# Performance work log

Hardware: AMD Instinct MI355X
Metric: run time of the kernel (lower is better)

## Reference

```python
import jax, jax.numpy as jnp
import numpy as np

B, C, W, H = 16, 512, 32, 32
CQ = C // 2
WSCALE = 0.05  # keep energy logits in a sane range for softmax


def setup_inputs() -> dict:
    key = jax.random.key(0)
    ks = jax.random.split(key, 6)
    return {
        "x": jax.random.normal(ks[0], (B, C, W, H), dtype=jnp.float32),
        "Wq": jax.random.normal(ks[1], (CQ, C), dtype=jnp.float32) * WSCALE,
        "bq": jnp.zeros((CQ,), dtype=jnp.float32),
        "Wk": jax.random.normal(ks[2], (CQ, C), dtype=jnp.float32) * WSCALE,
        "bk": jnp.zeros((CQ,), dtype=jnp.float32),
        "Wv": jax.random.normal(ks[3], (C, C), dtype=jnp.float32) * WSCALE,
        "bv": jnp.zeros((C,), dtype=jnp.float32),
        "Wa": jax.random.normal(ks[4], (1, C), dtype=jnp.float32) * WSCALE,
        "ba": jnp.zeros((1,), dtype=jnp.float32),
        "gamma": jax.random.normal(ks[5], (1,), dtype=jnp.float32) * 0.1,
    }


def reference(x, Wq, bq, Wk, bk, Wv, bv, Wa, ba, gamma):
    b, c, w, h = x.shape
    n = w * h
    xf = x.reshape(b, c, n)  # flatten spatial: B,C,N
    # 1x1 convs == per-position channel matmuls
    q = jnp.einsum('oc,bcn->bon', Wq, xf) + bq[None, :, None]  # B,C/2,N
    k = jnp.einsum('oc,bcn->bon', Wk, xf) + bk[None, :, None]  # B,C/2,N
    v = jnp.einsum('oc,bcn->bon', Wv, xf) + bv[None, :, None]  # B,C,N
    # energy[b,i,j] = <q[:, i], k[:, j]>  (unscaled, single head)
    energy = jnp.einsum('bci,bcj->bij', q, k)  # B,N,N
    attn = jax.nn.softmax(energy, axis=-1)
    # out[b,c,i] = sum_j v[b,c,j] * attn[b,i,j]
    out = jnp.einsum('bcj,bij->bci', v, attn).reshape(b, c, w, h)
    # agnostic gating: 1x1 conv C->1 + sigmoid, gate = 1 - sigmoid
    ag = jax.nn.sigmoid(jnp.einsum('oc,bchw->bohw', Wa, out) + ba[None, :, None, None])
    out_A = out * (1.0 - ag)
    out_final = gamma[0] * out + x
    return (out_final, out_A)
```

## Files before the change

### kernel.cpp

```cpp
#include <hip/hip_runtime.h>
#include <hip/hip_bf16.h>
#include <math.h>

#define B 16
#define C 512
#define CQ 256
#define N 1024

typedef short bf16x8 __attribute__((ext_vector_type(8)));
typedef _Float16 f16x8 __attribute__((ext_vector_type(8)));
typedef float f32x4 __attribute__((ext_vector_type(4)));
typedef unsigned short ushort;

__device__ __forceinline__ unsigned short f2bf(float f) {
    __hip_bfloat16 h = __float2bfloat16(f);
    return *(unsigned short*)&h;
}
__device__ __forceinline__ ushort f2h(float f) {
    _Float16 h = (_Float16)f;
    return *(ushort*)&h;
}
__device__ __forceinline__ float h2f(ushort u) {
    _Float16 h = *(_Float16*)&u;
    return (float)h;
}
__device__ __forceinline__ f16x8 as_h(bf16x8 v) {
    union { bf16x8 s; f16x8 h; } u; u.s = v; return u.h;
}

__device__ __forceinline__ void gload16(void* lds, const void* g) {
    __builtin_amdgcn_global_load_lds(
        (const __attribute__((address_space(1))) void*)g,
        (__attribute__((address_space(3))) void*)lds, 16, 0, 0);
}

__device__ __forceinline__ void barrier_lgkm() {
    asm volatile("s_waitcnt lgkmcnt(0)" ::: "memory");
    __builtin_amdgcn_s_barrier();
    __builtin_amdgcn_sched_barrier(0);
}

template<int OUT_MODE, int BIAS_MODE, int XSWZ, int DT>
__global__ __launch_bounds__(256) void gemm128s(
    const ushort* __restrict__ A, long long sA,
    const ushort* __restrict__ BT, long long sB,
    void* __restrict__ Ch, long long sC,
    const float* __restrict__ bias, int K, int Ncols)
{
    __shared__ __align__(16) ushort As[128 * 128];
    __shared__ __align__(16) ushort Bs[128 * 128];

    int bx, by, bz;
    if constexpr (XSWZ) {
        const int lin  = blockIdx.x + gridDim.x * (blockIdx.y + gridDim.y * blockIdx.z);
        const int xcd  = lin & 7;
        const int slot = lin >> 3;
        bz = xcd + 8 * (slot >> 5);
        const int wxy = slot & 31;
        bx = wxy % gridDim.x;
        by = wxy / gridDim.x;
    } else {
        bx = blockIdx.x; by = blockIdx.y; bz = blockIdx.z;
    }

    const int tid  = threadIdx.x;
    const int lane = tid & 63;
    const int w    = tid >> 6;
    const int wr   = (w >> 1) * 64;
    const int wc   = (w & 1) * 64;
    const int fr   = lane & 15;
    const int ko2  = (lane >> 4) * 16;

    const int brow = by * 128;
    const int bcol = bx * 128;
    const size_t K2 = (size_t)K * 2;

    const char* Ab = (const char*)(A  + (size_t)bz * sA + (size_t)brow * K);
    const char* Bb = (const char*)(BT + (size_t)bz * sB + (size_t)bcol * K);

    const int sr = tid >> 4;
    const int ss = (tid & 15) * 16;

    f32x4 acc[4][4] = {};

    for (int k0 = 0; k0 < K; k0 += 128) {
#pragma unroll
        for (int p = 0; p < 8; ++p) {
            const int row = p * 16 + sr;
            const size_t so = (size_t)row * K2 + (size_t)k0 * 2
                            + (size_t)(ss ^ ((row & 15) << 4));
            gload16((char*)As + p * 4096 + tid * 16, Ab + so);
            gload16((char*)Bs + p * 4096 + tid * 16, Bb + so);
        }
        __syncthreads();
#pragma unroll
        for (int k32 = 0; k32 < 4; ++k32) {
            const int kswz = (k32 * 64 + ko2) ^ (fr << 4);
            bf16x8 ah[4], bh[4];
#pragma unroll
            for (int m = 0; m < 4; ++m)
                ah[m] = *(const bf16x8*)((const char*)As + (wr + m * 16 + fr) * 256 + kswz);
#pragma unroll
            for (int n = 0; n < 4; ++n)
                bh[n] = *(const bf16x8*)((const char*)Bs + (wc + n * 16 + fr) * 256 + kswz);
            if constexpr (DT == 1) {
#pragma unroll
                for (int m = 0; m < 4; ++m)
#pragma unroll
                    for (int n = 0; n < 4; ++n)
                        acc[m][n] = __builtin_amdgcn_mfma_f32_16x16x32_f16(
                            as_h(ah[m]), as_h(bh[n]), acc[m][n], 0, 0, 0);
            } else {
#pragma unroll
                for (int m = 0; m < 4; ++m)
#pragma unroll
                    for (int n = 0; n < 4; ++n)
                        acc[m][n] = __builtin_amdgcn_mfma_f32_16x16x32_bf16(
                            ah[m], bh[n], acc[m][n], 0, 0, 0);
            }
        }
        __syncthreads();
    }

    const int crow = brow + wr + (lane >> 4) * 4;
    const int ccol = bcol + wc + fr;
    const size_t cbase = (size_t)bz * sC;
#pragma unroll
    for (int m = 0; m < 4; ++m) {
#pragma unroll
        for (int n = 0; n < 4; ++n) {
            float cb = (BIAS_MODE == 2) ? bias[ccol + n * 16] : 0.f;
#pragma unroll
            for (int r = 0; r < 4; ++r) {
                int row = crow + m * 16 + r;
                int col = ccol + n * 16;
                float vv = acc[m][n][r];
                if (BIAS_MODE == 1) vv += bias[row];
                if (BIAS_MODE == 2) vv += cb;
                size_t idx = cbase + (size_t)row * Ncols + col;
                if (OUT_MODE == 0)      ((float*)Ch)[idx]  = vv;
                else if (OUT_MODE == 1) ((ushort*)Ch)[idx] = f2bf(vv);
                else                    ((ushort*)Ch)[idx] = f2h(vv);
            }
        }
    }
}

__global__ __launch_bounds__(512, 2) void fused_attn(
    const ushort* __restrict__ qk, const ushort* __restrict__ vmat,
    const float* __restrict__ Wa, const float* __restrict__ ba,
    const float* __restrict__ gamma, const float* __restrict__ x,
    float* __restrict__ dout)
{
    __shared__ __align__(16) char lds[149504];
    __shared__ float redbuf[2][2][4][32];
    __shared__ float redA[8][64];
    __shared__ float agL[64];

    const int tid  = threadIdx.x;
    const int lane = tid & 63;
    const int w    = tid >> 6;
    const int g    = w >> 2;
    const int wg4  = w & 3;
    const int fr   = lane & 15;
    const int il0  = (lane >> 4) * 4;
    const int ko2  = (lane >> 4) * 16;

    const int wgid = blockIdx.x + gridDim.x * blockIdx.y;
    const int nid  = (wgid & 7) * 32 + (wgid >> 3);
    const int b    = nid >> 4;
    const int i0   = (nid & 15) * 64;

    const char* qkB = (const char*)qk + (size_t)b * N * 1024;
    const char* vB  = (const char*)vmat + (size_t)b * C * N * 2;

    const int srow = tid >> 4;
    const int ssg  = (tid & 15) * 16;

    f16x8 a_h[2][2][4];
#pragma unroll
    for (int ks0 = 0; ks0 < 2; ++ks0)
#pragma unroll
        for (int m = 0; m < 2; ++m) {
            const char* qr = qkB + (size_t)(i0 + g * 32 + m * 16 + fr) * 1024
                           + ks0 * 256 + (lane >> 4) * 16;
#pragma unroll
            for (int k32 = 0; k32 < 4; ++k32)
                a_h[ks0][m][k32] = *(const f16x8*)(qr + k32 * 64);
        }

    auto stageK = [&](int s) {
        const int jt_  = s & 7;
        const int ks0_ = s >> 3;
        char* dst = lds + (s & 3) * 32768;
#pragma unroll
        for (int p = 0; p < 4; ++p) {
            const int row = p * 32 + srow;
            const size_t so = (size_t)(jt_ * 128 + row) * 1024 + 512
                            + (size_t)(ks0_ * 256)
                            + (size_t)(ssg ^ ((row & 15) << 4));
            gload16(dst + p * 8192 + tid * 16, qkB + so);
        }
    };

    f32x4 acc[16][2];
#pragma unroll
    for (int jt = 0; jt < 16; ++jt)
#pragma unroll
        for (int m = 0; m < 2; ++m)
            acc[jt][m] = (f32x4){0.f, 0.f, 0.f, 0.f};

    stageK(0);
    stageK(1);

#pragma unroll
    for (int s = 0; s < 16; ++s) {
        if (s + 2 < 16) stageK(s + 2);
        if (s < 14)       asm volatile("s_waitcnt vmcnt(8)" ::: "memory");
        else if (s == 14) asm volatile("s_waitcnt vmcnt(4)" ::: "memory");
        else              asm volatile("s_waitcnt vmcnt(0)" ::: "memory");
        __builtin_amdgcn_s_barrier();
        __builtin_amdgcn_sched_barrier(0);
        const char* kb = lds + (s & 3) * 32768;
        const int ks0 = s >> 3;
#pragma unroll
        for (int sub = 0; sub < 2; ++sub) {
            const int jrow = sub * 64 + wg4 * 16 + fr;
            const int rb   = jrow * 256;
            const int jidx = (s & 7) * 2 + sub;
#pragma unroll
            for (int k32 = 0; k32 < 4; ++k32) {
                const int kswz = (k32 * 64 + ko2) ^ (fr << 4);
                f16x8 b_h = *(const f16x8*)(kb + rb + kswz);
#pragma unroll
                for (int m = 0; m < 2; ++m)
                    acc[jidx][m] = __builtin_amdgcn_mfma_f32_16x16x32_f16(
                        a_h[ks0][m][k32], b_h, acc[jidx][m], 0, 0, 0);
            }
        }
    }

    auto stageV = [&](int j) {
        char* dst = lds + (j & 1) * 65536;
#pragma unroll
        for (int p = 0; p < 8; ++p) {
            const int ch = p * 512 + tid;
            const int row = ch >> 3;
            const int sg  = (ch & 7) * 16;
            const size_t so = (size_t)row * (N * 2) + (size_t)(j * 128)
                            + (size_t)(sg ^ ((row & 7) << 4));
            gload16(dst + ch * 16, vB + so);
        }
    };
    stageV(0);

    float mx[2][4];
#pragma unroll
    for (int m = 0; m < 2; ++m)
#pragma unroll
        for (int r = 0; r < 4; ++r) {
            float v = acc[0][m][r];
#pragma unroll
            for (int jt = 1; jt < 16; ++jt) v = fmaxf(v, acc[jt][m][r]);
            mx[m][r] = v;
        }
#pragma unroll
    for (int off = 1; off < 16; off <<= 1)
#pragma unroll
        for (int m = 0; m < 2; ++m)
#pragma unroll
            for (int r = 0; r < 4; ++r)
                mx[m][r] = fmaxf(mx[m][r], __shfl_xor(mx[m][r], off, 64));
    if (fr == 0) {
#pragma unroll
        for (int m = 0; m < 2; ++m)
#pragma unroll
            for (int r = 0; r < 4; ++r)
                redbuf[0][g][wg4][m * 16 + il0 + r] = mx[m][r];
    }
    barrier_lgkm();
#pragma unroll
    for (int m = 0; m < 2; ++m)
#pragma unroll
        for (int r = 0; r < 4; ++r) {
            const int row = m * 16 + il0 + r;
            mx[m][r] = fmaxf(fmaxf(redbuf[0][g][0][row], redbuf[0][g][1][row]),
                             fmaxf(redbuf[0][g][2][row], redbuf[0][g][3][row]));
        }

    float sm[2][4] = {};
#pragma unroll
    for (int jt = 0; jt < 16; ++jt)
#pragma unroll
        for (int m = 0; m < 2; ++m) {
            f32x4 e;
#pragma unroll
            for (int r = 0; r < 4; ++r) {
                e[r] = __expf(acc[jt][m][r] - mx[m][r]);
                sm[m][r] += e[r];
            }
            acc[jt][m] = e;
        }
#pragma unroll
    for (int off = 1; off < 16; off <<= 1)
#pragma unroll
        for (int m = 0; m < 2; ++m)
#pragma unroll
            for (int r = 0; r < 4; ++r)
                sm[m][r] += __shfl_xor(sm[m][r], off, 64);
    if (fr == 0) {
#pragma unroll
        for (int m = 0; m < 2; ++m)
#pragma unroll
            for (int r = 0; r < 4; ++r)
                redbuf[1][g][wg4][m * 16 + il0 + r] = sm[m][r];
    }
    barrier_lgkm();
#pragma unroll
    for (int m = 0; m < 2; ++m)
#pragma unroll
        for (int r = 0; r < 4; ++r) {
            const int row = m * 16 + il0 + r;
            float s = redbuf[1][g][0][row] + redbuf[1][g][1][row]
                    + redbuf[1][g][2][row] + redbuf[1][g][3][row];
            mx[m][r] = 1.f / s;
        }

    char* pPb = lds + 131072;
    f32x4 apv[4][4] = {};

#pragma unroll
    for (int jt = 0; jt < 16; ++jt) {
        ushort* pS = (ushort*)(pPb + (jt & 1) * 9216);
#pragma unroll
        for (int m = 0; m < 2; ++m) {
            const int lr = g * 32 + m * 16 + il0;
#pragma unroll
            for (int r = 0; r < 4; ++r)
                pS[(lr + r) * 72 + wg4 * 16 + fr] = f2h(acc[jt][m][r] * mx[m][r]);
        }
        asm volatile("s_waitcnt vmcnt(0) lgkmcnt(0)" ::: "memory");
        __builtin_amdgcn_s_barrier();
        __builtin_amdgcn_sched_barrier(0);
        if (jt + 1 < 16) stageV(jt + 1);
        const char* vb = lds + (jt & 1) * 65536;
#pragma unroll
        for (int k32 = 0; k32 < 2; ++k32) {
            f16x8 af[4], bf[4];
#pragma unroll
            for (int cf = 0; cf < 4; ++cf) {
                const int row = w * 64 + cf * 16 + fr;
                const int kb  = (k32 * 64 + ko2) ^ ((fr & 7) << 4);
                af[cf] = *(const f16x8*)(vb + row * 128 + kb);
            }
#pragma unroll
            for (int f = 0; f < 4; ++f)
                bf[f] = *(const f16x8*)((const char*)pS
                        + (f * 16 + fr) * 144 + k32 * 64 + ko2);
#pragma unroll
            for (int cf = 0; cf < 4; ++cf)
#pragma unroll
                for (int f = 0; f < 4; ++f)
                    apv[cf][f] = __builtin_amdgcn_mfma_f32_16x16x32_f16(
                        af[cf], bf[f], apv[cf][f], 0, 0, 0);
        }
    }

    float pg[4] = {0.f, 0.f, 0.f, 0.f};
#pragma unroll
    for (int cf = 0; cf < 4; ++cf)
#pragma unroll
        for (int r = 0; r < 4; ++r) {
            const float wv = Wa[w * 64 + cf * 16 + il0 + r];
#pragma unroll
            for (int f = 0; f < 4; ++f)
                pg[f] += wv * apv[cf][f][r];
        }
#pragma unroll
    for (int off = 16; off < 64; off <<= 1)
#pragma unroll
        for (int f = 0; f < 4; ++f)
            pg[f] += __shfl_xor(pg[f], off, 64);
    if (lane < 16) {
#pragma unroll
        for (int f = 0; f < 4; ++f)
            redA[w][f * 16 + fr] = pg[f];
    }
    barrier_lgkm();
    if (tid < 64) {
        float s = ba[0];
#pragma unroll
        for (int k = 0; k < 8; ++k) s += redA[k][tid];
        agL[tid] = 1.f / (1.f + __expf(-s));
    }

    const size_t BCN = (size_t)B * C * N;
    const float gmm = gamma[0];
    float* oS = (float*)lds;

#pragma unroll
    for (int h = 0; h < 2; ++h) {
#pragma unroll
        for (int cf = 0; cf < 4; ++cf) {
            const int crow = w * 64 + cf * 16 + il0;
#pragma unroll
            for (int f = 0; f < 2; ++f) {
                const int col = f * 16 + fr;
#pragma unroll
                for (int r = 0; r < 4; ++r)
                    oS[(crow + r) * 33 + col] = apv[cf][2 * h + f][r];
            }
        }
        barrier_lgkm();
#pragma unroll
        for (int p = 0; p < 8; ++p) {
            const int ch  = p * 512 + tid;
            const int row = ch >> 3;
            const int sg  = ch & 7;
            const int ib  = h * 32 + sg * 4;
            f32x4 o = *(const f32x4*)&oS[row * 33 + sg * 4];
            const size_t idx = ((size_t)b * C + row) * N + i0 + ib;
            f32x4 xv = *(const f32x4*)&x[idx];
            f32x4 of, oa;
#pragma unroll
            for (int q = 0; q < 4; ++q) {
                of[q] = gmm * o[q] + xv[q];
                oa[q] = o[q] * (1.f - agL[ib + q]);
            }
            *(f32x4*)&dout[idx]       = of;
            *(f32x4*)&dout[BCN + idx] = oa;
        }
        barrier_lgkm();
    }
}

__global__ void transpose_x_f16(const float* __restrict__ x,
                                ushort* __restrict__ xT) {
    __shared__ float t[32][33];
    int b  = blockIdx.z;
    int c0 = blockIdx.y * 32;
    int n0 = blockIdx.x * 32;
    int tid = threadIdx.x;
    int tx = tid & 31;
    int ty = tid >> 5;
#pragma unroll
    for (int r = 0; r < 4; ++r)
        t[ty + r * 8][tx] = x[(size_t)b * C * N + (size_t)(c0 + ty + r * 8) * N + n0 + tx];
    __syncthreads();
#pragma unroll
    for (int r = 0; r < 4; ++r) {
        float v = t[tx][ty + r * 8];
        size_t idx = (size_t)b * N * C + (size_t)(n0 + ty + r * 8) * C + c0 + tx;
        xT[idx] = f2h(v);
    }
}

__global__ void prep_weights(const float* __restrict__ Wq, const float* __restrict__ Wk,
                             const float* __restrict__ Wv,
                             const float* __restrict__ bq, const float* __restrict__ bk,
                             ushort* __restrict__ Wqk, ushort* __restrict__ Wv16,
                             float* __restrict__ bqk) {
    int i = blockIdx.x * 256 + threadIdx.x;
    if (i < CQ * C) {
        Wqk[i]          = f2h(Wq[i]);
        Wqk[CQ * C + i] = f2h(Wk[i]);
    }
    if (i < C * C) Wv16[i] = f2h(Wv[i]);
    if (i < 512) bqk[i] = (i < CQ) ? bq[i] : bk[i - CQ];
}

extern "C" void kernel_launch(void* const* d_in, const int* in_sizes, int n_in,
                              void* d_out, int out_size, void* d_ws, size_t ws_size,
                              hipStream_t stream) {
    const float* x     = (const float*)d_in[0];
    const float* Wq    = (const float*)d_in[1];
    const float* bq    = (const float*)d_in[2];
    const float* Wk    = (const float*)d_in[3];
    const float* bk    = (const float*)d_in[4];
    const float* Wv    = (const float*)d_in[5];
    const float* bv    = (const float*)d_in[6];
    const float* Wa    = (const float*)d_in[7];
    const float* ba    = (const float*)d_in[8];
    const float* gamma = (const float*)d_in[9];
    float* out = (float*)d_out;

    const size_t MB = 1048576;
    char* ws = (char*)d_ws;
    ushort* v_     = (ushort*)(ws);
    ushort* qkT    = (ushort*)(ws + 16 * MB);
    ushort* Wqk    = (ushort*)(ws + 48 * MB);
    ushort* Wv16   = (ushort*)(ws + 48 * MB + 524288);
    float*  bqk    = (float*)(ws + 49 * MB);
    ushort* xT     = (ushort*)(ws + 80 * MB);
    const size_t need = 96 * MB;
    if (ws_size < need) return;

    dim3 blk(256);
    transpose_x_f16<<<dim3(N / 32, C / 32, B), blk, 0, stream>>>(x, xT);
    prep_weights<<<dim3(C * C / 256), blk, 0, stream>>>(
        Wq, Wk, Wv, bq, bk, Wqk, Wv16, bqk);

    gemm128s<3, 2, 1, 1><<<dim3(4, 8, B), blk, 0, stream>>>(
        xT, (long long)N * C, Wqk, 0,
        qkT, (long long)N * 512, bqk, C, 512);
    gemm128s<3, 1, 1, 1><<<dim3(8, 4, B), blk, 0, stream>>>(
        Wv16, 0, xT, (long long)N * C,
        v_, (long long)C * N, bv, C, N);
    fused_attn<<<dim3(16, 16), dim3(512), 0, stream>>>(
        qkT, v_, Wa, ba, gamma, x, out);
}
```

Measured before the change: 98.13 us.

## Merge QK and V projection GEMMs into one launch; add MFMA priority and early x prefetch

The two separate projection GEMM launches become one 1024-block kernel that interleaves QK and V tiles, picking operands at runtime from the block index. This removes one launch and its tail, and lets both GEMMs share the machine at the same time. The attention kernel also raises wave priority around its MFMA loops with s_setprio, and loads the residual x values before the LDS transpose in the epilogue so that latency overlaps. In exchange, the merged GEMM uses runtime branching on bias mode and strides, and the early x loads hold more registers.

```diff
diff --git a/kernel.cpp b/kernel.cpp
--- a/kernel.cpp
+++ b/kernel.cpp
@@ -40,28 +40,39 @@
     __builtin_amdgcn_sched_barrier(0);
 }
 
-template<int OUT_MODE, int BIAS_MODE, int XSWZ, int DT>
-__global__ __launch_bounds__(256) void gemm128s(
-    const ushort* __restrict__ A, long long sA,
-    const ushort* __restrict__ BT, long long sB,
-    void* __restrict__ Ch, long long sC,
-    const float* __restrict__ bias, int K, int Ncols)
+__global__ __launch_bounds__(256) void gemm_dual(
+    const ushort* __restrict__ xT, const ushort* __restrict__ Wqk,
+    const ushort* __restrict__ Wv16,
+    ushort* __restrict__ qkT, ushort* __restrict__ v_,
+    const float* __restrict__ bqk, const float* __restrict__ bv)
 {
     __shared__ __align__(16) ushort As[128 * 128];
     __shared__ __align__(16) ushort Bs[128 * 128];
 
-    int bx, by, bz;
-    if constexpr (XSWZ) {
-        const int lin  = blockIdx.x + gridDim.x * (blockIdx.y + gridDim.y * blockIdx.z);
-        const int xcd  = lin & 7;
-        const int slot = lin >> 3;
-        bz = xcd + 8 * (slot >> 5);
-        const int wxy = slot & 31;
-        bx = wxy % gridDim.x;
-        by = wxy / gridDim.x;
+    const int lin  = blockIdx.x;
+    const int half = lin & 1;
+    const int slot = lin >> 1;
+    const int xcd  = slot & 7;
+    const int s2   = slot >> 3;
+    const int bz   = xcd + 8 * (s2 >> 5);
+    const int wxy  = s2 & 31;
+    const int bx   = half ? (wxy & 7) : (wxy & 3);
+    const int by   = half ? (wxy >> 3) : (wxy >> 2);
+
+    const ushort* A;  long long sA;
+    const ushort* BT; long long sB;
+    ushort* Ch;       long long sC;
+    const float* bias; int bias_mode; int Ncols;
+    if (half == 0) {
+        A = xT;   sA = (long long)N * C;  BT = Wqk;  sB = 0;
+        Ch = qkT; sC = (long long)N * 512;
+        bias = bqk; bias_mode = 2; Ncols = 512;
     } else {
-        bx = blockIdx.x; by = blockIdx.y; bz = blockIdx.z;
-    }
+        A = Wv16; sA = 0;                 BT = xT;   sB = (long long)N * C;
+        Ch = v_;  sC = (long long)C * N;
+        bias = bv;  bias_mode = 1; Ncols = N;
+    }
+    const int K = C;
 
     const int tid  = threadIdx.x;
     const int lane = tid & 63;
@@ -103,21 +114,12 @@
 #pragma unroll
             for (int n = 0; n < 4; ++n)
                 bh[n] = *(const bf16x8*)((const char*)Bs + (wc + n * 16 + fr) * 256 + kswz);
-            if constexpr (DT == 1) {
-#pragma unroll
-                for (int m = 0; m < 4; ++m)
-#pragma unroll
-                    for (int n = 0; n < 4; ++n)
-                        acc[m][n] = __builtin_amdgcn_mfma_f32_16x16x32_f16(
-                            as_h(ah[m]), as_h(bh[n]), acc[m][n], 0, 0, 0);
-            } else {
-#pragma unroll
-                for (int m = 0; m < 4; ++m)
-#pragma unroll
-                    for (int n = 0; n < 4; ++n)
-                        acc[m][n] = __builtin_amdgcn_mfma_f32_16x16x32_bf16(
-                            ah[m], bh[n], acc[m][n], 0, 0, 0);
-            }
+#pragma unroll
+            for (int m = 0; m < 4; ++m)
+#pragma unroll
+                for (int n = 0; n < 4; ++n)
+                    acc[m][n] = __builtin_amdgcn_mfma_f32_16x16x32_f16(
+                        as_h(ah[m]), as_h(bh[n]), acc[m][n], 0, 0, 0);
         }
         __syncthreads();
     }
@@ -129,18 +131,14 @@
     for (int m = 0; m < 4; ++m) {
 #pragma unroll
         for (int n = 0; n < 4; ++n) {
-            float cb = (BIAS_MODE == 2) ? bias[ccol + n * 16] : 0.f;
+            const float cb = (bias_mode == 2) ? bias[ccol + n * 16] : 0.f;
 #pragma unroll
             for (int r = 0; r < 4; ++r) {
-                int row = crow + m * 16 + r;
-                int col = ccol + n * 16;
-                float vv = acc[m][n][r];
-                if (BIAS_MODE == 1) vv += bias[row];
-                if (BIAS_MODE == 2) vv += cb;
-                size_t idx = cbase + (size_t)row * Ncols + col;
-                if (OUT_MODE == 0)      ((float*)Ch)[idx]  = vv;
-                else if (OUT_MODE == 1) ((ushort*)Ch)[idx] = f2bf(vv);
-                else                    ((ushort*)Ch)[idx] = f2h(vv);
+                const int row = crow + m * 16 + r;
+                const int col = ccol + n * 16;
+                float vv = acc[m][n][r]
+                         + ((bias_mode == 1) ? bias[row] : cb);
+                Ch[cbase + (size_t)row * Ncols + col] = f2h(vv);
             }
         }
     }
@@ -223,6 +221,7 @@
         __builtin_amdgcn_sched_barrier(0);
         const char* kb = lds + (s & 3) * 32768;
         const int ks0 = s >> 3;
+        __builtin_amdgcn_s_setprio(1);
 #pragma unroll
         for (int sub = 0; sub < 2; ++sub) {
             const int jrow = sub * 64 + wg4 * 16 + fr;
@@ -238,6 +237,7 @@
                         a_h[ks0][m][k32], b_h, acc[jidx][m], 0, 0, 0);
             }
         }
+        __builtin_amdgcn_s_setprio(0);
     }
 
     auto stageV = [&](int j) {
@@ -357,12 +357,14 @@
             for (int f = 0; f < 4; ++f)
                 bf[f] = *(const f16x8*)((const char*)pS
                         + (f * 16 + fr) * 144 + k32 * 64 + ko2);
+            __builtin_amdgcn_s_setprio(1);
 #pragma unroll
             for (int cf = 0; cf < 4; ++cf)
 #pragma unroll
                 for (int f = 0; f < 4; ++f)
                     apv[cf][f] = __builtin_amdgcn_mfma_f32_16x16x32_f16(
                         af[cf], bf[f], apv[cf][f], 0, 0, 0);
+            __builtin_amdgcn_s_setprio(0);
         }
     }
 
@@ -400,6 +402,16 @@
 
 #pragma unroll
     for (int h = 0; h < 2; ++h) {
+        f32x4 xv[8];
+#pragma unroll
+        for (int p = 0; p < 8; ++p) {
+            const int ch  = p * 512 + tid;
+            const int row = ch >> 3;
+            const int sg  = ch & 7;
+            const int ib  = h * 32 + sg * 4;
+            const size_t idx = ((size_t)b * C + row) * N + i0 + ib;
+            xv[p] = *(const f32x4*)&x[idx];
+        }
 #pragma unroll
         for (int cf = 0; cf < 4; ++cf) {
             const int crow = w * 64 + cf * 16 + il0;
@@ -420,11 +432,10 @@
             const int ib  = h * 32 + sg * 4;
             f32x4 o = *(const f32x4*)&oS[row * 33 + sg * 4];
             const size_t idx = ((size_t)b * C + row) * N + i0 + ib;
-            f32x4 xv = *(const f32x4*)&x[idx];
             f32x4 of, oa;
 #pragma unroll
             for (int q = 0; q < 4; ++q) {
-                of[q] = gmm * o[q] + xv[q];
+                of[q] = gmm * o[q] + xv[p][q];
                 oa[q] = o[q] * (1.f - agL[ib + q]);
             }
             *(f32x4*)&dout[idx]       = of;
@@ -500,12 +511,9 @@
     prep_weights<<<dim3(C * C / 256), blk, 0, stream>>>(
         Wq, Wk, Wv, bq, bk, Wqk, Wv16, bqk);
 
-    gemm128s<3, 2, 1, 1><<<dim3(4, 8, B), blk, 0, stream>>>(
-        xT, (long long)N * C, Wqk, 0,
-        qkT, (long long)N * 512, bqk, C, 512);
-    gemm128s<3, 1, 1, 1><<<dim3(8, 4, B), blk, 0, stream>>>(
-        Wv16, 0, xT, (long long)N * C,
-        v_, (long long)C * N, bv, C, N);
+    gemm_dual<<<dim3(1024), blk, 0, stream>>>(
+        xT, Wqk, Wv16, qkT, v_, bqk, bv);
+
     fused_attn<<<dim3(16, 16), dim3(512), 0, stream>>>(
         qkT, v_, Wa, ba, gamma, x, out);
 }
```

Measured after the change: 114.1 us. +16.2%, slower.
